# Performance work log

Hardware: AMD Instinct MI355X
Metric: run time of the kernel (lower is better)

## Reference

```python
import jax, jax.numpy as jnp
import numpy as np
import math

B, S, D = 8, 2048, 1024

def setup_inputs() -> dict:
    key = jax.random.key(0)
    ks = jax.random.split(key, 9)
    scale = 1.0 / math.sqrt(D)
    Q = jax.random.normal(ks[0], (B, S, D), dtype=jnp.float32)
    K = jax.random.normal(ks[1], (B, S, D), dtype=jnp.float32)
    V = jax.random.normal(ks[2], (B, S, D), dtype=jnp.float32)
    Wq = jax.random.normal(ks[3], (D, D), dtype=jnp.float32) * scale
    Wk = jax.random.normal(ks[4], (D, D), dtype=jnp.float32) * scale
    Wv = jax.random.normal(ks[5], (D, D), dtype=jnp.float32) * scale
    bq = jnp.zeros((D,), dtype=jnp.float32)
    bk = jnp.zeros((D,), dtype=jnp.float32)
    bv = jnp.zeros((D,), dtype=jnp.float32)
    # causal mask, broadcast over batch: [1, S, S]
    mask = jnp.tril(jnp.ones((S, S), dtype=jnp.int32))[None, :, :]
    return {"Q": Q, "K": K, "V": V, "Wq": Wq, "Wk": Wk, "Wv": Wv,
            "bq": bq, "bk": bk, "bv": bv, "mask": mask}

def reference(Q, K, V, Wq, Wk, Wv, bq, bk, bv, mask):
    d_model = Q.shape[-1]
    q = jnp.einsum('bsd,de->bse', Q, Wq) + bq
    k = jnp.einsum('bsd,de->bse', K, Wk) + bk
    v = jnp.einsum('bsd,de->bse', V, Wv) + bv
    scores = jnp.einsum('bqd,bkd->bqk', q, k) / math.sqrt(d_model)  # [B,S,S]
    scores = jnp.where(mask == 0, jnp.float32(-1e9), scores)
    weights = jax.nn.softmax(scores, axis=-1)
    out = jnp.einsum('bqk,bkd->bqd', weights, v)
    return out
```

## Files before the change

### kernel.cpp

```cpp
#include <hip/hip_runtime.h>
#include <hip/hip_bf16.h>

#define Bb 8
#define Ss 2048
#define Dd 1024

typedef short bf16x8 __attribute__((ext_vector_type(8)));
typedef float f32x4  __attribute__((ext_vector_type(4)));

__device__ __forceinline__ short f2bf(float f) {
  union { __hip_bfloat16 h; short s; } u;
  u.h = __float2bfloat16(f);
  return u.s;
}
__device__ __forceinline__ float bf2f(short s) {
  union { unsigned int u; float f; } v;
  v.u = ((unsigned int)(unsigned short)s) << 16;
  return v.f;
}

__device__ __forceinline__ int swz(int row, int slot) {
  return row * 64 + (((slot ^ row) & 7) << 3);
}
__device__ __forceinline__ int swzf(int row, int slot) {
  return row * 64 + (((slot ^ row) & 15) << 2);
}

__device__ __forceinline__ void gld16(const void* g, void* l) {
  __builtin_amdgcn_global_load_lds((const __attribute__((address_space(1))) void*)g,
                                   (__attribute__((address_space(3))) void*)l, 16, 0, 0);
}

__device__ __forceinline__ void stage_glds(const short* __restrict__ src, int ld,
                                           short* lds, int tid) {
  int w = tid >> 6;
#pragma unroll
  for (int it = 0; it < 4; ++it) {
    int u = it * 256 + tid;
    int r = u >> 3;
    int ssrc = (u ^ r) & 7;
    gld16(src + (size_t)r * ld + ssrc * 8, lds + (size_t)(it * 256 + w * 64) * 8);
  }
}

__device__ __forceinline__ void stage_glds_f32(const float* __restrict__ src, int ld,
                                               float* lds, int tid) {
  int w = tid >> 6;
#pragma unroll
  for (int it = 0; it < 8; ++it) {
    int u = it * 256 + tid;
    int r = u >> 4;
    int ssrc = (u ^ r) & 15;
    gld16(src + (size_t)r * ld + ssrc * 4, lds + (size_t)(it * 256 + w * 64) * 4);
  }
}

__device__ __forceinline__ void mfma_tile(const short* ldsA, const short* ldsB,
                                          f32x4 acc[4][4], int wm, int wn, int lr, int lk) {
#pragma unroll
  for (int c = 0; c < 2; ++c) {
    bf16x8 afr[4], bfr[4];
#pragma unroll
    for (int m = 0; m < 4; ++m)
      afr[m] = *(const bf16x8*)&ldsA[swz(wm * 64 + m * 16 + lr, c * 4 + lk)];
#pragma unroll
    for (int n = 0; n < 4; ++n)
      bfr[n] = *(const bf16x8*)&ldsB[swz(wn * 64 + n * 16 + lr, c * 4 + lk)];
#pragma unroll
    for (int m = 0; m < 4; ++m)
#pragma unroll
      for (int n = 0; n < 4; ++n)
        acc[m][n] = __builtin_amdgcn_mfma_f32_16x16x32_bf16(afr[m], bfr[n], acc[m][n], 0, 0, 0);
  }
}

__device__ __forceinline__ void mfma_tile_f32A(const float* ldsA, const short* ldsB,
                                               f32x4 acc[4][4], int wm, int wn,
                                               int lr, int lk) {
#pragma unroll
  for (int c = 0; c < 2; ++c) {
    bf16x8 afr[4], bfr[4];
#pragma unroll
    for (int m = 0; m < 4; ++m) {
      int r = wm * 64 + m * 16 + lr;
      int s0 = c * 8 + lk * 2;
      f32x4 a0 = *(const f32x4*)&ldsA[swzf(r, s0)];
      f32x4 a1 = *(const f32x4*)&ldsA[swzf(r, s0 + 1)];
      bf16x8 h;
      h[0] = f2bf(a0[0]); h[1] = f2bf(a0[1]); h[2] = f2bf(a0[2]); h[3] = f2bf(a0[3]);
      h[4] = f2bf(a1[0]); h[5] = f2bf(a1[1]); h[6] = f2bf(a1[2]); h[7] = f2bf(a1[3]);
      afr[m] = h;
    }
#pragma unroll
    for (int n = 0; n < 4; ++n)
      bfr[n] = *(const bf16x8*)&ldsB[swz(wn * 64 + n * 16 + lr, c * 4 + lk)];
#pragma unroll
    for (int m = 0; m < 4; ++m)
#pragma unroll
      for (int n = 0; n < 4; ++n)
        acc[m][n] = __builtin_amdgcn_mfma_f32_16x16x32_bf16(afr[m], bfr[n], acc[m][n], 0, 0, 0);
  }
}

__global__ void wcast_kernel(const float* __restrict__ Wq, const float* __restrict__ Wk,
                             const float* __restrict__ Wv,
                             short* __restrict__ WtQ, short* __restrict__ WtK,
                             short* __restrict__ WtV) {
  int z = blockIdx.z;
  const float* W = (z == 0) ? Wq : (z == 1) ? Wk : Wv;
  short* Wt      = (z == 0) ? WtQ : (z == 1) ? WtK : WtV;
  __shared__ float tile[32][33];
  int r0 = blockIdx.y * 32, c0 = blockIdx.x * 32;
  int tx = threadIdx.x, ty = threadIdx.y;
#pragma unroll
  for (int ii = 0; ii < 4; ++ii) {
    int r = ty * 4 + ii;
    tile[r][tx] = W[(size_t)(r0 + r) * Dd + c0 + tx];
  }
  __syncthreads();
#pragma unroll
  for (int ii = 0; ii < 4; ++ii) {
    int c = ty * 4 + ii;
    Wt[(size_t)(c0 + c) * Dd + r0 + tx] = f2bf(tile[tx][c]);
  }
}

__launch_bounds__(256, 3)
__global__ void proj_kernel(const float* __restrict__ Q, const float* __restrict__ Kin,
                            const float* __restrict__ V,
                            const short* __restrict__ WtQ, const short* __restrict__ WtK,
                            const short* __restrict__ WtV,
                            const float* __restrict__ bq, const float* __restrict__ bk,
                            const float* __restrict__ bv,
                            short* __restrict__ qb, short* __restrict__ kb,
                            short* __restrict__ vT) {
  __shared__ float ldsA[128 * 64];
  __shared__ short ldsB[128 * 64];
  int z = blockIdx.y;
  const float* A    = (z == 0) ? Q : (z == 1) ? Kin : V;
  const short* W    = (z == 0) ? WtQ : (z == 1) ? WtK : WtV;
  const float* bias = (z == 0) ? bq : (z == 1) ? bk : bv;

  int r = blockIdx.x;
  int x = r & 7;
  int s = r >> 3;
  int nblk = s & 7;
  int mblk = x + 8 * (s >> 3);
  int m0 = mblk * 128;
  int n0 = nblk * 128;

  int tid = threadIdx.x;
  int lane = tid & 63, w = tid >> 6;
  int wm = w >> 1, wn = w & 1;
  int lr = lane & 15, lk = lane >> 4;

  const float* Ab = A + (size_t)m0 * Dd;
  const short* Wb = W + (size_t)n0 * Dd;

  f32x4 acc[4][4] = {};
  for (int k0 = 0; k0 < Dd; k0 += 64) {
    __syncthreads();
    stage_glds_f32(Ab + k0, Dd, ldsA, tid);
    stage_glds(Wb + k0, Dd, ldsB, tid);
    __syncthreads();
    mfma_tile_f32A(ldsA, ldsB, acc, wm, wn, lr, lk);
  }

  if (z < 2) {
    short* out = (z == 0) ? qb : kb;
#pragma unroll
    for (int m = 0; m < 4; ++m)
#pragma unroll
      for (int n = 0; n < 4; ++n) {
        int col = n0 + wn * 64 + n * 16 + lr;
        float bv_ = bias[col];
        int rbase = m0 + wm * 64 + m * 16 + lk * 4;
#pragma unroll
        for (int rr = 0; rr < 4; ++rr)
          out[(size_t)(rbase + rr) * Dd + col] = f2bf(acc[m][n][rr] + bv_);
      }
  } else {
#pragma unroll
    for (int m = 0; m < 4; ++m)
#pragma unroll
      for (int n = 0; n < 4; ++n) {
        int col = n0 + wn * 64 + n * 16 + lr;
        float bv_ = bias[col];
        int rbase = m0 + wm * 64 + m * 16 + lk * 4;
        int bidx = rbase / Ss;
        int s0 = rbase & (Ss - 1);
        short4 h;
        h.x = f2bf(acc[m][n][0] + bv_);
        h.y = f2bf(acc[m][n][1] + bv_);
        h.z = f2bf(acc[m][n][2] + bv_);
        h.w = f2bf(acc[m][n][3] + bv_);
        *(short4*)&vT[(size_t)bidx * Dd * Ss + (size_t)col * Ss + s0] = h;
      }
  }
}

__launch_bounds__(256, 4)
__global__ void score_kernel(const short* __restrict__ qb, const short* __restrict__ kb,
                             short* __restrict__ SP) {
  int d = blockIdx.x;
  int b = d & 7;
  int sidx = d >> 3;
  int i = (int)((sqrtf(8.f * sidx + 1.f) - 1.f) * 0.5f);
  while ((i + 1) * (i + 2) / 2 <= sidx) ++i;
  while (i * (i + 1) / 2 > sidx) --i;
  int j = sidx - i * (i + 1) / 2;

  __shared__ short ldsA[128 * 64];
  __shared__ short ldsB[128 * 64];
  int tid = threadIdx.x;
  int lane = tid & 63, w = tid >> 6;
  int wm = w >> 1, wn = w & 1;
  int lr = lane & 15, lk = lane >> 4;

  const short* Abase = qb + (size_t)b * Ss * Dd + (size_t)i * 128 * Dd;
  const short* Bbase = kb + (size_t)b * Ss * Dd + (size_t)j * 128 * Dd;

  f32x4 acc[4][4] = {};
  for (int k0 = 0; k0 < Dd; k0 += 64) {
    __syncthreads();
    stage_glds(Abase + k0, Dd, ldsA, tid);
    stage_glds(Bbase + k0, Dd, ldsB, tid);
    __syncthreads();
    mfma_tile(ldsA, ldsB, acc, wm, wn, lr, lk);
  }

  short* srow = SP + (size_t)b * Ss * Ss;
#pragma unroll
  for (int m = 0; m < 4; ++m)
#pragma unroll
    for (int n = 0; n < 4; ++n) {
      int colg = j * 128 + wn * 64 + n * 16 + lr;
      int rbase = i * 128 + wm * 64 + m * 16 + lk * 4;
#pragma unroll
      for (int rr = 0; rr < 4; ++rr) {
        int rowg = rbase + rr;
        float sv = acc[m][n][rr] * 0.03125f;
        if (colg > rowg) sv = -1e9f;
        srow[(size_t)rowg * Ss + colg] = f2bf(sv);
      }
    }
}

__global__ void softmax_kernel(short* __restrict__ SP) {
  int row = blockIdx.x;
  int b = row >> 11;
  int q = row & (Ss - 1);
  int L = ((q >> 7) + 1) << 7;
  short* srow = SP + (size_t)b * Ss * Ss + (size_t)q * Ss;
  int tid = threadIdx.x;
  int lane = tid & 63, w = tid >> 6;
  int c8 = tid * 8;
  bool act = c8 < L;

  float v[8];
  float mx = -3.0e38f;
  if (act) {
    bf16x8 hv = *(const bf16x8*)&srow[c8];
#pragma unroll
    for (int j2 = 0; j2 < 8; ++j2) {
      v[j2] = bf2f(hv[j2]);
      mx = fmaxf(mx, v[j2]);
    }
  }
  __shared__ float red[8];
#pragma unroll
  for (int off = 32; off; off >>= 1) mx = fmaxf(mx, __shfl_xor(mx, off));
  if (lane == 0) red[w] = mx;
  __syncthreads();
  mx = fmaxf(fmaxf(red[0], red[1]), fmaxf(red[2], red[3]));

  float sum = 0.f;
  if (act) {
#pragma unroll
    for (int j2 = 0; j2 < 8; ++j2) {
      v[j2] = __expf(v[j2] - mx);
      sum += v[j2];
    }
  }
#pragma unroll
  for (int off = 32; off; off >>= 1) sum += __shfl_xor(sum, off);
  if (lane == 0) red[4 + w] = sum;
  __syncthreads();
  sum = red[4] + red[5] + red[6] + red[7];
  float inv = 1.0f / sum;

  if (act) {
    bf16x8 ho;
#pragma unroll
    for (int j2 = 0; j2 < 8; ++j2) ho[j2] = f2bf(v[j2] * inv);
    *(bf16x8*)&srow[c8] = ho;
  }
}

__launch_bounds__(256, 4)
__global__ void pv_kernel(const short* __restrict__ SP, const short* __restrict__ vT,
                          float* __restrict__ out) {
  int d = blockIdx.x;
  int b = d & 7;
  int s = d >> 3;
  int i = s >> 3;
  int dblk = s & 7;

  __shared__ short ldsA[128 * 64];
  __shared__ short ldsB[128 * 64];
  int tid = threadIdx.x;
  int lane = tid & 63, w = tid >> 6;
  int wm = w >> 1, wn = w & 1;
  int lr = lane & 15, lk = lane >> 4;

  const short* Abase = SP + (size_t)b * Ss * Ss + (size_t)i * 128 * Ss;
  const short* Bbase = vT + (size_t)b * Dd * Ss + (size_t)dblk * 128 * Ss;
  int KL = (i + 1) * 128;

  f32x4 acc[4][4] = {};
  for (int k0 = 0; k0 < KL; k0 += 64) {
    __syncthreads();
    stage_glds(Abase + k0, Ss, ldsA, tid);
    stage_glds(Bbase + k0, Ss, ldsB, tid);
    __syncthreads();
    mfma_tile(ldsA, ldsB, acc, wm, wn, lr, lk);
  }

#pragma unroll
  for (int m = 0; m < 4; ++m)
#pragma unroll
    for (int n = 0; n < 4; ++n) {
      int colg = dblk * 128 + wn * 64 + n * 16 + lr;
      int rbase = i * 128 + wm * 64 + m * 16 + lk * 4;
#pragma unroll
      for (int rr = 0; rr < 4; ++rr)
        out[(size_t)b * Ss * Dd + (size_t)(rbase + rr) * Dd + colg] = acc[m][n][rr];
    }
}

extern "C" void kernel_launch(void* const* d_in, const int* in_sizes, int n_in,
                              void* d_out, int out_size, void* d_ws, size_t ws_size,
                              hipStream_t stream) {
  const float* Q  = (const float*)d_in[0];
  const float* K  = (const float*)d_in[1];
  const float* V  = (const float*)d_in[2];
  const float* Wq = (const float*)d_in[3];
  const float* Wk = (const float*)d_in[4];
  const float* Wv = (const float*)d_in[5];
  const float* bq = (const float*)d_in[6];
  const float* bk = (const float*)d_in[7];
  const float* bv = (const float*)d_in[8];
  float* out = (float*)d_out;

  char* ws = (char*)d_ws;
  size_t off = 0;
  short* WtQ = (short*)(ws + off); off += (size_t)Dd * Dd * 2;
  short* WtK = (short*)(ws + off); off += (size_t)Dd * Dd * 2;
  short* WtV = (short*)(ws + off); off += (size_t)Dd * Dd * 2;
  short* qb  = (short*)(ws + off); off += (size_t)Bb * Ss * Dd * 2;
  short* kb  = (short*)(ws + off); off += (size_t)Bb * Ss * Dd * 2;
  short* vT  = (short*)(ws + off); off += (size_t)Bb * Ss * Dd * 2;
  short* SP  = (short*)(ws + off); off += (size_t)Bb * Ss * Ss * 2;
  (void)ws_size; (void)in_sizes; (void)n_in; (void)out_size;

  wcast_kernel<<<dim3(32, 32, 3), dim3(32, 8), 0, stream>>>(Wq, Wk, Wv, WtQ, WtK, WtV);
  proj_kernel<<<dim3(1024, 3), 256, 0, stream>>>(Q, K, V, WtQ, WtK, WtV, bq, bk, bv,
                                                 qb, kb, vT);
  score_kernel<<<dim3(1088), 256, 0, stream>>>(qb, kb, SP);
  softmax_kernel<<<dim3(Bb * Ss), 256, 0, stream>>>(SP);
  pv_kernel<<<dim3(1024), 256, 0, stream>>>(SP, vT, out);
}
```

Measured before the change: 288.4 us.

## Load fp32 activations directly from global into registers in projection kernel

```diff
diff --git a/kernel.cpp b/kernel.cpp
--- a/kernel.cpp
+++ b/kernel.cpp
@@ -21,9 +21,6 @@
 
 __device__ __forceinline__ int swz(int row, int slot) {
   return row * 64 + (((slot ^ row) & 7) << 3);
-}
-__device__ __forceinline__ int swzf(int row, int slot) {
-  return row * 64 + (((slot ^ row) & 15) << 2);
 }
 
 __device__ __forceinline__ void gld16(const void* g, void* l) {
@@ -43,18 +40,6 @@
   }
 }
 
-__device__ __forceinline__ void stage_glds_f32(const float* __restrict__ src, int ld,
-                                               float* lds, int tid) {
-  int w = tid >> 6;
-#pragma unroll
-  for (int it = 0; it < 8; ++it) {
-    int u = it * 256 + tid;
-    int r = u >> 4;
-    int ssrc = (u ^ r) & 15;
-    gld16(src + (size_t)r * ld + ssrc * 4, lds + (size_t)(it * 256 + w * 64) * 4);
-  }
-}
-
 __device__ __forceinline__ void mfma_tile(const short* ldsA, const short* ldsB,
                                           f32x4 acc[4][4], int wm, int wn, int lr, int lk) {
 #pragma unroll
@@ -63,34 +48,6 @@
 #pragma unroll
     for (int m = 0; m < 4; ++m)
       afr[m] = *(const bf16x8*)&ldsA[swz(wm * 64 + m * 16 + lr, c * 4 + lk)];
-#pragma unroll
-    for (int n = 0; n < 4; ++n)
-      bfr[n] = *(const bf16x8*)&ldsB[swz(wn * 64 + n * 16 + lr, c * 4 + lk)];
-#pragma unroll
-    for (int m = 0; m < 4; ++m)
-#pragma unroll
-      for (int n = 0; n < 4; ++n)
-        acc[m][n] = __builtin_amdgcn_mfma_f32_16x16x32_bf16(afr[m], bfr[n], acc[m][n], 0, 0, 0);
-  }
-}
-
-__device__ __forceinline__ void mfma_tile_f32A(const float* ldsA, const short* ldsB,
-                                               f32x4 acc[4][4], int wm, int wn,
-                                               int lr, int lk) {
-#pragma unroll
-  for (int c = 0; c < 2; ++c) {
-    bf16x8 afr[4], bfr[4];
-#pragma unroll
-    for (int m = 0; m < 4; ++m) {
-      int r = wm * 64 + m * 16 + lr;
-      int s0 = c * 8 + lk * 2;
-      f32x4 a0 = *(const f32x4*)&ldsA[swzf(r, s0)];
-      f32x4 a1 = *(const f32x4*)&ldsA[swzf(r, s0 + 1)];
-      bf16x8 h;
-      h[0] = f2bf(a0[0]); h[1] = f2bf(a0[1]); h[2] = f2bf(a0[2]); h[3] = f2bf(a0[3]);
-      h[4] = f2bf(a1[0]); h[5] = f2bf(a1[1]); h[6] = f2bf(a1[2]); h[7] = f2bf(a1[3]);
-      afr[m] = h;
-    }
 #pragma unroll
     for (int n = 0; n < 4; ++n)
       bfr[n] = *(const bf16x8*)&ldsB[swz(wn * 64 + n * 16 + lr, c * 4 + lk)];
@@ -125,7 +82,7 @@
   }
 }
 
-__launch_bounds__(256, 3)
+__launch_bounds__(256, 4)
 __global__ void proj_kernel(const float* __restrict__ Q, const float* __restrict__ Kin,
                             const float* __restrict__ V,
                             const short* __restrict__ WtQ, const short* __restrict__ WtK,
@@ -134,7 +91,6 @@
                             const float* __restrict__ bv,
                             short* __restrict__ qb, short* __restrict__ kb,
                             short* __restrict__ vT) {
-  __shared__ float ldsA[128 * 64];
   __shared__ short ldsB[128 * 64];
   int z = blockIdx.y;
   const float* A    = (z == 0) ? Q : (z == 1) ? Kin : V;
@@ -154,16 +110,46 @@
   int wm = w >> 1, wn = w & 1;
   int lr = lane & 15, lk = lane >> 4;
 
-  const float* Ab = A + (size_t)m0 * Dd;
   const short* Wb = W + (size_t)n0 * Dd;
+  const float* Arow[4];
+#pragma unroll
+  for (int m = 0; m < 4; ++m)
+    Arow[m] = A + (size_t)(m0 + wm * 64 + m * 16 + lr) * Dd + lk * 8;
 
   f32x4 acc[4][4] = {};
-  for (int k0 = 0; k0 < Dd; k0 += 64) {
-    __syncthreads();
-    stage_glds_f32(Ab + k0, Dd, ldsA, tid);
-    stage_glds(Wb + k0, Dd, ldsB, tid);
-    __syncthreads();
-    mfma_tile_f32A(ldsA, ldsB, acc, wm, wn, lr, lk);
+
+  stage_glds(Wb, Dd, ldsB, tid);
+  __syncthreads();
+
+  for (int t = 0; t < 16; ++t) {
+    int k0 = t * 64;
+#pragma unroll
+    for (int c = 0; c < 2; ++c) {
+      bf16x8 afr[4], bfr[4];
+#pragma unroll
+      for (int m = 0; m < 4; ++m) {
+        const float* g = Arow[m] + k0 + c * 32;
+        f32x4 a0 = *(const f32x4*)g;
+        f32x4 a1 = *(const f32x4*)(g + 4);
+        bf16x8 h;
+        h[0] = f2bf(a0[0]); h[1] = f2bf(a0[1]); h[2] = f2bf(a0[2]); h[3] = f2bf(a0[3]);
+        h[4] = f2bf(a1[0]); h[5] = f2bf(a1[1]); h[6] = f2bf(a1[2]); h[7] = f2bf(a1[3]);
+        afr[m] = h;
+      }
+#pragma unroll
+      for (int n = 0; n < 4; ++n)
+        bfr[n] = *(const bf16x8*)&ldsB[swz(wn * 64 + n * 16 + lr, c * 4 + lk)];
+#pragma unroll
+      for (int m = 0; m < 4; ++m)
+#pragma unroll
+        for (int n = 0; n < 4; ++n)
+          acc[m][n] = __builtin_amdgcn_mfma_f32_16x16x32_bf16(afr[m], bfr[n], acc[m][n], 0, 0, 0);
+    }
+    if (t + 1 < 16) {
+      __syncthreads();
+      stage_glds(Wb + (t + 1) * 64, Dd, ldsB, tid);
+      __syncthreads();
+    }
   }
 
   if (z < 2) {
```

After: 527.5 us. +82.9%, slower.
